# Kernel optimization log

Hardware: AMD Instinct MI355X
Metric: run time of the kernel (lower is better)

## Reference

```python
import jax, jax.numpy as jnp
import numpy as np

B, P, D, C = 1024, 4, 512, 128  # batch, parts, feat_dim, num_classes


def setup_inputs() -> dict:
    key = jax.random.key(0)
    k1, k2 = jax.random.split(key)
    # scale 0.05 keeps dot products O(1) so exp() stays in fp32 range
    inputs = jax.random.normal(k1, (B, P, D), dtype=jnp.float32) * 0.05
    targets = jax.random.randint(k2, (B,), 0, C, dtype=jnp.int64)
    return {"inputs": inputs, "targets": targets}


def _npairs_loss(inputs, targets):
    b, p, d = inputs.shape
    n = b * p
    X = inputs.reshape(n, d)
    t = jnp.repeat(targets, p)              # (n,) class label per row
    parts = jnp.tile(jnp.arange(p), b)      # (n,) part id per row
    prod = X @ X.T                          # (n, n) similarities

    sc = t[:, None] == t[None, :]           # same class
    sp = parts[:, None] == parts[None, :]   # same attention part
    s_sadc = (~sc) & sp
    s_dasc = sc & (~sp)
    s_dadc = (~sc) & (~sp)

    e_pos = jnp.exp(prod)                   # exp(neg) terms
    e_neg = jnp.exp(-prod)                  # exp(-pos) terms

    def group_loss(pos_mask, neg_mask):
        # sum_i sum_{j in pos_i} log(1 + sum_{k in neg_i} exp(prod[i,k] - prod[i,j]))
        # = sum log1p(S_i * exp(-prod[i,j])) with S_i = sum_{k in neg_i} exp(prod[i,k])
        S = jnp.sum(jnp.where(neg_mask, e_pos, 0.0), axis=1)        # (n,)
        terms = jnp.where(pos_mask, jnp.log1p(S[:, None] * e_neg), 0.0)
        return jnp.sum(terms)

    loss_sadc = group_loss(s_sadc, s_dadc)
    loss_dasc = group_loss(s_dasc, s_dadc)
    # NOTE: original returns loss_sadc twice and never uses loss_sasc (bug kept for fidelity)
    return (loss_sadc + loss_sadc + loss_dasc) / n


def reference(inputs, targets):
    return _npairs_loss(inputs, targets)
```

## Files before the change

kernel.cpp:

```cpp
#include <hip/hip_runtime.h>
#include <stdint.h>

#define GLOBAL_AS __attribute__((address_space(1)))
#define LDS_AS    __attribute__((address_space(3)))

typedef __attribute__((ext_vector_type(8))) __bf16 bf16x8;
typedef __attribute__((ext_vector_type(4))) float  f32x4;

static_assert(sizeof(bf16x8) == 16, "bf16x8 must be 16B");

constexpr int N  = 4096;
constexpr int DK = 512;


__global__ void k_convert(const float* __restrict__ X, __bf16* __restrict__ Xb) {
    int idx = blockIdx.x * blockDim.x + threadIdx.x;
    const float4* s = (const float4*)X;
    float4 a = s[2 * idx + 0];
    float4 b = s[2 * idx + 1];
    bf16x8 o;
    o[0] = (__bf16)a.x; o[1] = (__bf16)a.y; o[2] = (__bf16)a.z; o[3] = (__bf16)a.w;
    o[4] = (__bf16)b.x; o[5] = (__bf16)b.y; o[6] = (__bf16)b.z; o[7] = (__bf16)b.w;
    *(bf16x8*)(Xb + 8 * idx) = o;
}

__global__ void k_cls(const int* __restrict__ tbuf, int* __restrict__ cls) {
    __shared__ int is64;
    int t = threadIdx.x;
    if (t == 0) is64 = 1;
    __syncthreads();
    if (t < 512 && tbuf[2 * t + 1] != 0) is64 = 0;
    __syncthreads();
    int idx = is64 ? (2 * t) : t;
    int v = tbuf[idx];
    cls[4 * t + 0] = v;
    cls[4 * t + 1] = v;
    cls[4 * t + 2] = v;
    cls[4 * t + 3] = v;
}

__launch_bounds__(256, 2)
__global__ void k_main(const __bf16* __restrict__ Xb, const int* __restrict__ cls,
                       float* __restrict__ partials) {
    __shared__ __align__(16) __bf16 As[2][128 * 64];
    __shared__ __align__(16) __bf16 Bs[2][128 * 64];
    __shared__ float accS[128], accP[128], accE[128], accW[128];
    __shared__ float accSc[128], accPc[128], accEc[128], accWc[128];
    __shared__ int rowcls[128], colcls[128];

    const int tid  = threadIdx.x;
    const int lane = tid & 63;
    const int wid  = tid >> 6;

    const int bid = blockIdx.x;
    int rt = (int)((sqrtf(8.0f * (float)bid + 1.0f) - 1.0f) * 0.5f);
    while (((rt + 1) * (rt + 2)) / 2 <= bid) ++rt;
    while ((rt * (rt + 1)) / 2 > bid) --rt;
    const int g  = bid - (rt * (rt + 1)) / 2;
    const int i0 = rt * 128;
    const int j0 = g * 128;
    const bool offdiag = (rt != g);

    if (tid < 128) {
        rowcls[tid] = cls[i0 + tid];
        colcls[tid] = cls[j0 + tid];
        accS[tid] = 0.f;  accP[tid] = 0.f;  accE[tid] = 0.f;  accW[tid] = 0.f;
        accSc[tid] = 0.f; accPc[tid] = 0.f; accEc[tid] = 0.f; accWc[tid] = 0.f;
    }

    const int wr = wid >> 1;
    const int wc = wid & 1;

    f32x4 acc[4][4] = {};

    const char* xb   = (const char*)Xb;
    const int   srow = tid >> 3;
    const int   skb  = (tid & 7) * 16;
    const int ldsOff = wid * 1024;

    const int rA   = lane & 15;
    const int kgrp = lane >> 4;

#define STAGE(buf, kt)                                                                     \
    {                                                                                      \
        const size_t kb0 = (size_t)(kt) * 128;                                             \
        char* AsB = (char*)(&As[(buf)][0]);                                                \
        char* BsB = (char*)(&Bs[(buf)][0]);                                                \
        _Pragma("unroll")                                                                  \
        for (int t = 0; t < 4; ++t) {                                                      \
            __builtin_amdgcn_global_load_lds(                                              \
                (const GLOBAL_AS void*)(xb + (size_t)(i0 + t * 32 + srow) * 1024 + kb0 + skb), \
                (LDS_AS void*)(AsB + t * 4096 + ldsOff), 16, 0, 0);                        \
            __builtin_amdgcn_global_load_lds(                                              \
                (const GLOBAL_AS void*)(xb + (size_t)(j0 + t * 32 + srow) * 1024 + kb0 + skb), \
                (LDS_AS void*)(BsB + t * 4096 + ldsOff), 16, 0, 0);                        \
        }                                                                                  \
    }

    STAGE(0, 0);
    __syncthreads();

    int cur = 0;
#pragma unroll
    for (int kt = 0; kt < DK / 64; ++kt) {
        if (kt < DK / 64 - 1) STAGE(cur ^ 1, kt + 1);
        const char* AsB = (const char*)(&As[cur][0]);
        const char* BsB = (const char*)(&Bs[cur][0]);
#pragma unroll
        for (int kk = 0; kk < 2; ++kk) {
            const int koff = kk * 64 + kgrp * 16;
            bf16x8 af[4], bg[4];
#pragma unroll
            for (int m = 0; m < 4; ++m)
                af[m] = *(const bf16x8*)(AsB + (wr * 64 + m * 16 + rA) * 128 + koff);
#pragma unroll
            for (int n = 0; n < 4; ++n)
                bg[n] = *(const bf16x8*)(BsB + (wc * 64 + n * 16 + rA) * 128 + koff);
#pragma unroll
            for (int m = 0; m < 4; ++m)
#pragma unroll
                for (int n = 0; n < 4; ++n)
                    acc[m][n] = __builtin_amdgcn_mfma_f32_16x16x32_bf16(af[m], bg[n],
                                                                        acc[m][n], 0, 0, 0);
        }
        if (kt < DK / 64 - 1) {
            __syncthreads();
            cur ^= 1;
        }
    }
#undef STAGE

    const int pj = lane & 3;
    int cjv[4];
#pragma unroll
    for (int n = 0; n < 4; ++n) cjv[n] = colcls[wc * 64 + n * 16 + rA];
    float cS[4] = {0.f, 0.f, 0.f, 0.f};
    float cP[4] = {0.f, 0.f, 0.f, 0.f};
    float cE[4] = {0.f, 0.f, 0.f, 0.f};
    float cW[4] = {0.f, 0.f, 0.f, 0.f};

#pragma unroll
    for (int m = 0; m < 4; ++m) {
        const int rbase = wr * 64 + m * 16 + kgrp * 4;
        int ci[4];
#pragma unroll
        for (int r = 0; r < 4; ++r) ci[r] = rowcls[rbase + r];
        float sS[4] = {0.f, 0.f, 0.f, 0.f};
        float sP[4] = {0.f, 0.f, 0.f, 0.f};
        float sE[4] = {0.f, 0.f, 0.f, 0.f};
        float sW[4] = {0.f, 0.f, 0.f, 0.f};
#pragma unroll
        for (int n = 0; n < 4; ++n) {
            const int cj = cjv[n];
#pragma unroll
            for (int r = 0; r < 4; ++r) {
                const float p  = acc[m][n][r];
                const float ep = __expf(p);
                const bool sc = (ci[r] == cj);
                const bool sp = (r == pj);
                const bool dadc = (!sc && !sp);
                if (dadc) { sS[r] += ep; cS[n] += ep; }
                const float w = (!sc && sp) ? 2.f : ((sc && !sp) ? 1.f : 0.f);
                sP[r] += w * p;  sE[r] += w * ep;  sW[r] += w;
                cP[n] += w * p;  cE[n] += w * ep;  cW[n] += w;
            }
        }
#pragma unroll
        for (int r = 0; r < 4; ++r) {
            float vS = sS[r], vP = sP[r], vE = sE[r], vW = sW[r];
#pragma unroll
            for (int off = 1; off < 16; off <<= 1) {
                vS += __shfl_xor(vS, off);
                vP += __shfl_xor(vP, off);
                vE += __shfl_xor(vE, off);
                vW += __shfl_xor(vW, off);
            }
            if (rA == 0) {
                const int row = rbase + r;
                atomicAdd(&accS[row], vS);
                atomicAdd(&accP[row], vP);
                atomicAdd(&accE[row], vE);
                atomicAdd(&accW[row], vW);
            }
        }
    }

    if (offdiag) {
#pragma unroll
        for (int n = 0; n < 4; ++n) {
            float vS = cS[n], vP = cP[n], vE = cE[n], vW = cW[n];
            vS += __shfl_xor(vS, 16); vS += __shfl_xor(vS, 32);
            vP += __shfl_xor(vP, 16); vP += __shfl_xor(vP, 32);
            vE += __shfl_xor(vE, 16); vE += __shfl_xor(vE, 32);
            vW += __shfl_xor(vW, 16); vW += __shfl_xor(vW, 32);
            if (kgrp == 0) {
                const int col = wc * 64 + n * 16 + rA;
                atomicAdd(&accSc[col], vS);
                atomicAdd(&accPc[col], vP);
                atomicAdd(&accEc[col], vE);
                atomicAdd(&accWc[col], vW);
            }
        }
    }

    __syncthreads();
    if (tid < 128) {
        float4 o = make_float4(accS[tid], accP[tid], accE[tid], accW[tid]);
        ((float4*)partials)[(size_t)(i0 + tid) * 32 + g] = o;
        if (offdiag) {
            float4 oc = make_float4(accSc[tid], accPc[tid], accEc[tid], accWc[tid]);
            ((float4*)partials)[(size_t)(j0 + tid) * 32 + rt] = oc;
        }
    }
}

__global__ void k_rowloss(const float* __restrict__ partials, float* __restrict__ blockSums) {
    __shared__ float red[16];
    const int tid = threadIdx.x;
    const int sub = tid & 15;
    const int row = blockIdx.x * 16 + (tid >> 4);

    const float4* p = ((const float4*)partials) + (size_t)row * 32;
    float4 a = p[sub];
    float4 b = p[sub + 16];
    float S = a.x + b.x, P = a.y + b.y, E = a.z + b.z, W = a.w + b.w;
#pragma unroll
    for (int off = 1; off < 16; off <<= 1) {
        S += __shfl_xor(S, off);
        P += __shfl_xor(P, off);
        E += __shfl_xor(E, off);
        W += __shfl_xor(W, off);
    }
    if (sub == 0) red[tid >> 4] = W * logf(S) - P + E / S;
    __syncthreads();
    if (tid == 0) {
        float s = 0.f;
#pragma unroll
        for (int r = 0; r < 16; ++r) s += red[r];
        blockSums[blockIdx.x] = s;
    }
}

__global__ void k_final2(const float* __restrict__ blockSums, float* __restrict__ out) {
    const int t = threadIdx.x;
    float v = blockSums[t] + blockSums[t + 64] + blockSums[t + 128] + blockSums[t + 192];
#pragma unroll
    for (int off = 1; off < 64; off <<= 1) v += __shfl_xor(v, off);
    if (t == 0) out[0] = v / (float)N;
}

extern "C" void kernel_launch(void* const* d_in, const int* in_sizes, int n_in,
                              void* d_out, int out_size, void* d_ws, size_t ws_size,
                              hipStream_t stream) {
    const float* X = (const float*)d_in[0];
    const int*   T = (const int*)d_in[1];
    float* out = (float*)d_out;

    char* ws = (char*)d_ws;
    __bf16* Xb     = (__bf16*)ws;
    int*    cls    = (int*)(ws + (size_t)4 * 1024 * 1024);
    float*  parts  = (float*)(ws + (size_t)4 * 1024 * 1024 + 16 * 1024);
    float*  bsums  = (float*)ws;

    hipLaunchKernelGGL(k_convert, dim3((N * DK / 8) / 256), dim3(256), 0, stream, X, Xb);
    hipLaunchKernelGGL(k_cls,     dim3(1),   dim3(1024), 0, stream, T, cls);
    hipLaunchKernelGGL(k_main,    dim3(528), dim3(256),  0, stream, Xb, cls, parts);
    hipLaunchKernelGGL(k_rowloss, dim3(256), dim3(256),  0, stream, parts, bsums);
    hipLaunchKernelGGL(k_final2,  dim3(1),   dim3(64),   0, stream, bsums, out);
}
```

Before: 56.65 us.

## Use 8-wave blocks with swizzled LDS tiles and merge class-label kernel into convert

```diff
diff --git a/kernel.cpp b/kernel.cpp
--- a/kernel.cpp
+++ b/kernel.cpp
@@ -13,7 +13,25 @@
 constexpr int DK = 512;
 
 
-__global__ void k_convert(const float* __restrict__ X, __bf16* __restrict__ Xb) {
+__global__ void k_convert(const float* __restrict__ X, __bf16* __restrict__ Xb,
+                          const int* __restrict__ tbuf, int* __restrict__ cls) {
+    if (blockIdx.x == 1024) {
+        __shared__ int is64;
+        const int t = threadIdx.x;
+        if (t == 0) is64 = 1;
+        __syncthreads();
+        if (tbuf[4 * t + 1] != 0 || tbuf[4 * t + 3] != 0) is64 = 0;
+        __syncthreads();
+        const int f = is64;
+#pragma unroll
+        for (int q = 0; q < 4; ++q) {
+            const int ti = 4 * t + q;
+            const int v = tbuf[f ? 2 * ti : ti];
+            cls[4 * ti + 0] = v; cls[4 * ti + 1] = v;
+            cls[4 * ti + 2] = v; cls[4 * ti + 3] = v;
+        }
+        return;
+    }
     int idx = blockIdx.x * blockDim.x + threadIdx.x;
     const float4* s = (const float4*)X;
     float4 a = s[2 * idx + 0];
@@ -24,33 +42,20 @@
     *(bf16x8*)(Xb + 8 * idx) = o;
 }
 
-__global__ void k_cls(const int* __restrict__ tbuf, int* __restrict__ cls) {
-    __shared__ int is64;
-    int t = threadIdx.x;
-    if (t == 0) is64 = 1;
-    __syncthreads();
-    if (t < 512 && tbuf[2 * t + 1] != 0) is64 = 0;
-    __syncthreads();
-    int idx = is64 ? (2 * t) : t;
-    int v = tbuf[idx];
-    cls[4 * t + 0] = v;
-    cls[4 * t + 1] = v;
-    cls[4 * t + 2] = v;
-    cls[4 * t + 3] = v;
-}
-
-__launch_bounds__(256, 2)
+__launch_bounds__(512, 4)
 __global__ void k_main(const __bf16* __restrict__ Xb, const int* __restrict__ cls,
                        float* __restrict__ partials) {
     __shared__ __align__(16) __bf16 As[2][128 * 64];
     __shared__ __align__(16) __bf16 Bs[2][128 * 64];
-    __shared__ float accS[128], accP[128], accE[128], accW[128];
-    __shared__ float accSc[128], accPc[128], accEc[128], accWc[128];
+    __shared__ float4 accR[4][128];
+    __shared__ float4 accC[2][128];
     __shared__ int rowcls[128], colcls[128];
 
     const int tid  = threadIdx.x;
     const int lane = tid & 63;
     const int wid  = tid >> 6;
+    const int wr   = wid >> 2;
+    const int wc   = wid & 3;
 
     const int bid = blockIdx.x;
     int rt = (int)((sqrtf(8.0f * (float)bid + 1.0f) - 1.0f) * 0.5f);
@@ -64,37 +69,31 @@
     if (tid < 128) {
         rowcls[tid] = cls[i0 + tid];
         colcls[tid] = cls[j0 + tid];
-        accS[tid] = 0.f;  accP[tid] = 0.f;  accE[tid] = 0.f;  accW[tid] = 0.f;
-        accSc[tid] = 0.f; accPc[tid] = 0.f; accEc[tid] = 0.f; accWc[tid] = 0.f;
-    }
-
-    const int wr = wid >> 1;
-    const int wc = wid & 1;
-
-    f32x4 acc[4][4] = {};
+    }
+
+    f32x4 acc[4][2] = {};
 
     const char* xb   = (const char*)Xb;
     const int   srow = tid >> 3;
-    const int   skb  = (tid & 7) * 16;
-    const int ldsOff = wid * 1024;
-
-    const int rA   = lane & 15;
-    const int kgrp = lane >> 4;
-
-#define STAGE(buf, kt)                                                                     \
-    {                                                                                      \
-        const size_t kb0 = (size_t)(kt) * 128;                                             \
-        char* AsB = (char*)(&As[(buf)][0]);                                                \
-        char* BsB = (char*)(&Bs[(buf)][0]);                                                \
-        _Pragma("unroll")                                                                  \
-        for (int t = 0; t < 4; ++t) {                                                      \
-            __builtin_amdgcn_global_load_lds(                                              \
-                (const GLOBAL_AS void*)(xb + (size_t)(i0 + t * 32 + srow) * 1024 + kb0 + skb), \
-                (LDS_AS void*)(AsB + t * 4096 + ldsOff), 16, 0, 0);                        \
-            __builtin_amdgcn_global_load_lds(                                              \
-                (const GLOBAL_AS void*)(xb + (size_t)(j0 + t * 32 + srow) * 1024 + kb0 + skb), \
-                (LDS_AS void*)(BsB + t * 4096 + ldsOff), 16, 0, 0);                        \
-        }                                                                                  \
+    const int   skb  = ((tid & 7) ^ (srow & 7)) * 16;
+    const int   ldst = wid * 1024;
+    const int   rA   = lane & 15;
+    const int   kgrp = lane >> 4;
+
+#define STAGE(buf, kt)                                                                         \
+    {                                                                                          \
+        const size_t kb0 = (size_t)(kt) * 128;                                                 \
+        char* AsB = (char*)(&As[(buf)][0]);                                                    \
+        char* BsB = (char*)(&Bs[(buf)][0]);                                                    \
+        _Pragma("unroll")                                                                      \
+        for (int t = 0; t < 2; ++t) {                                                          \
+            __builtin_amdgcn_global_load_lds(                                                  \
+                (const GLOBAL_AS void*)(xb + (size_t)(i0 + t * 64 + srow) * 1024 + kb0 + skb), \
+                (LDS_AS void*)(AsB + t * 8192 + ldst), 16, 0, 0);                              \
+            __builtin_amdgcn_global_load_lds(                                                  \
+                (const GLOBAL_AS void*)(xb + (size_t)(j0 + t * 64 + srow) * 1024 + kb0 + skb), \
+                (LDS_AS void*)(BsB + t * 8192 + ldst), 16, 0, 0);                              \
+        }                                                                                      \
     }
 
     STAGE(0, 0);
@@ -104,22 +103,26 @@
 #pragma unroll
     for (int kt = 0; kt < DK / 64; ++kt) {
         if (kt < DK / 64 - 1) STAGE(cur ^ 1, kt + 1);
-        const char* AsB = (const char*)(&As[cur][0]);
-        const char* BsB = (const char*)(&Bs[cur][0]);
+        const char* A_ = (const char*)(&As[cur][0]);
+        const char* B_ = (const char*)(&Bs[cur][0]);
 #pragma unroll
         for (int kk = 0; kk < 2; ++kk) {
-            const int koff = kk * 64 + kgrp * 16;
-            bf16x8 af[4], bg[4];
+            bf16x8 af[4];
+            bf16x8 bg[2];
+#pragma unroll
+            for (int m = 0; m < 4; ++m) {
+                const int r = wr * 64 + m * 16 + rA;
+                af[m] = *(const bf16x8*)(A_ + r * 128 + (((kk * 4 + kgrp) ^ (r & 7)) * 16));
+            }
+#pragma unroll
+            for (int n = 0; n < 2; ++n) {
+                const int r = wc * 32 + n * 16 + rA;
+                bg[n] = *(const bf16x8*)(B_ + r * 128 + (((kk * 4 + kgrp) ^ (r & 7)) * 16));
+            }
 #pragma unroll
             for (int m = 0; m < 4; ++m)
-                af[m] = *(const bf16x8*)(AsB + (wr * 64 + m * 16 + rA) * 128 + koff);
-#pragma unroll
-            for (int n = 0; n < 4; ++n)
-                bg[n] = *(const bf16x8*)(BsB + (wc * 64 + n * 16 + rA) * 128 + koff);
-#pragma unroll
-            for (int m = 0; m < 4; ++m)
-#pragma unroll
-                for (int n = 0; n < 4; ++n)
+#pragma unroll
+                for (int n = 0; n < 2; ++n)
                     acc[m][n] = __builtin_amdgcn_mfma_f32_16x16x32_bf16(af[m], bg[n],
                                                                         acc[m][n], 0, 0, 0);
         }
@@ -130,14 +133,11 @@
     }
 #undef STAGE
 
-    const int pj = lane & 3;
-    int cjv[4];
-#pragma unroll
-    for (int n = 0; n < 4; ++n) cjv[n] = colcls[wc * 64 + n * 16 + rA];
-    float cS[4] = {0.f, 0.f, 0.f, 0.f};
-    float cP[4] = {0.f, 0.f, 0.f, 0.f};
-    float cE[4] = {0.f, 0.f, 0.f, 0.f};
-    float cW[4] = {0.f, 0.f, 0.f, 0.f};
+    const int pj = rA & 3;
+    int cj[2];
+#pragma unroll
+    for (int n = 0; n < 2; ++n) cj[n] = colcls[wc * 32 + n * 16 + rA];
+    float cS[2] = {0.f, 0.f}, cP[2] = {0.f, 0.f}, cE[2] = {0.f, 0.f}, cW[2] = {0.f, 0.f};
 
 #pragma unroll
     for (int m = 0; m < 4; ++m) {
@@ -150,16 +150,14 @@
         float sE[4] = {0.f, 0.f, 0.f, 0.f};
         float sW[4] = {0.f, 0.f, 0.f, 0.f};
 #pragma unroll
-        for (int n = 0; n < 4; ++n) {
-            const int cj = cjv[n];
+        for (int n = 0; n < 2; ++n) {
 #pragma unroll
             for (int r = 0; r < 4; ++r) {
                 const float p  = acc[m][n][r];
                 const float ep = __expf(p);
-                const bool sc = (ci[r] == cj);
+                const bool sc = (ci[r] == cj[n]);
                 const bool sp = (r == pj);
-                const bool dadc = (!sc && !sp);
-                if (dadc) { sS[r] += ep; cS[n] += ep; }
+                if (!sc && !sp) { sS[r] += ep; cS[n] += ep; }
                 const float w = (!sc && sp) ? 2.f : ((sc && !sp) ? 1.f : 0.f);
                 sP[r] += w * p;  sE[r] += w * ep;  sW[r] += w;
                 cP[n] += w * p;  cE[n] += w * ep;  cW[n] += w;
@@ -175,40 +173,31 @@
                 vE += __shfl_xor(vE, off);
                 vW += __shfl_xor(vW, off);
             }
-            if (rA == 0) {
-                const int row = rbase + r;
-                atomicAdd(&accS[row], vS);
-                atomicAdd(&accP[row], vP);
-                atomicAdd(&accE[row], vE);
-                atomicAdd(&accW[row], vW);
-            }
-        }
-    }
-
-    if (offdiag) {
-#pragma unroll
-        for (int n = 0; n < 4; ++n) {
+            if (rA == 0) accR[wc][rbase + r] = make_float4(vS, vP, vE, vW);
+        }
+    }
+
+    {
+#pragma unroll
+        for (int n = 0; n < 2; ++n) {
             float vS = cS[n], vP = cP[n], vE = cE[n], vW = cW[n];
             vS += __shfl_xor(vS, 16); vS += __shfl_xor(vS, 32);
             vP += __shfl_xor(vP, 16); vP += __shfl_xor(vP, 32);
             vE += __shfl_xor(vE, 16); vE += __shfl_xor(vE, 32);
             vW += __shfl_xor(vW, 16); vW += __shfl_xor(vW, 32);
-            if (kgrp == 0) {
-                const int col = wc * 64 + n * 16 + rA;
-                atomicAdd(&accSc[col], vS);
-                atomicAdd(&accPc[col], vP);
-                atomicAdd(&accEc[col], vE);
-                atomicAdd(&accWc[col], vW);
-            }
+            if (kgrp == 0) accC[wr][wc * 32 + n * 16 + rA] = make_float4(vS, vP, vE, vW);
         }
     }
 
     __syncthreads();
     if (tid < 128) {
-        float4 o = make_float4(accS[tid], accP[tid], accE[tid], accW[tid]);
+        float4 a0 = accR[0][tid], a1 = accR[1][tid], a2 = accR[2][tid], a3 = accR[3][tid];
+        float4 o = make_float4(a0.x + a1.x + a2.x + a3.x, a0.y + a1.y + a2.y + a3.y,
+                               a0.z + a1.z + a2.z + a3.z, a0.w + a1.w + a2.w + a3.w);
         ((float4*)partials)[(size_t)(i0 + tid) * 32 + g] = o;
         if (offdiag) {
-            float4 oc = make_float4(accSc[tid], accPc[tid], accEc[tid], accWc[tid]);
+            float4 c0 = accC[0][tid], c1 = accC[1][tid];
+            float4 oc = make_float4(c0.x + c1.x, c0.y + c1.y, c0.z + c1.z, c0.w + c1.w);
             ((float4*)partials)[(size_t)(j0 + tid) * 32 + rt] = oc;
         }
     }
@@ -262,9 +251,8 @@
     float*  parts  = (float*)(ws + (size_t)4 * 1024 * 1024 + 16 * 1024);
     float*  bsums  = (float*)ws;
 
-    hipLaunchKernelGGL(k_convert, dim3((N * DK / 8) / 256), dim3(256), 0, stream, X, Xb);
-    hipLaunchKernelGGL(k_cls,     dim3(1),   dim3(1024), 0, stream, T, cls);
-    hipLaunchKernelGGL(k_main,    dim3(528), dim3(256),  0, stream, Xb, cls, parts);
-    hipLaunchKernelGGL(k_rowloss, dim3(256), dim3(256),  0, stream, parts, bsums);
-    hipLaunchKernelGGL(k_final2,  dim3(1),   dim3(64),   0, stream, bsums, out);
-}
+    hipLaunchKernelGGL(k_convert, dim3(1025), dim3(256), 0, stream, X, Xb, T, cls);
+    hipLaunchKernelGGL(k_main,    dim3(528),  dim3(512), 0, stream, Xb, cls, parts);
+    hipLaunchKernelGGL(k_rowloss, dim3(256),  dim3(256), 0, stream, parts, bsums);
+    hipLaunchKernelGGL(k_final2,  dim3(1),    dim3(64),  0, stream, bsums, out);
+}
```

After: 59.12 us. 1.04x slower.
